# Performance work log

Measured on AMD Instinct MI355X. Metric: run time of the kernel, lower is better.

Reference implementation:

```python
import jax, jax.numpy as jnp
import numpy as np

H = 256          # hidden_channels
NP, NJ, NC = 8192, 8192, 4096  # person / job_posting / company node counts
EA, EW, EP = 262144, 131072, 131072  # edge counts per relation


def _gcn(x_src, W, b, edge_index, num_src, num_dst):
    """Bipartite GCNConv: h = x_src @ W; out[dst] = sum_e norm_e * h[src_e] + b,
    norm = deg_out(src)^-1/2 * deg_in(dst)^-1/2 (symmetric GCN normalization)."""
    h = x_src @ W                                # [num_src, H]
    row, col = edge_index[0], edge_index[1]
    ones = jnp.ones(row.shape[0], dtype=h.dtype)
    deg_src = jax.ops.segment_sum(ones, row, num_segments=num_src)
    deg_dst = jax.ops.segment_sum(ones, col, num_segments=num_dst)
    dis_src = jnp.where(deg_src > 0, jax.lax.rsqrt(jnp.maximum(deg_src, 1e-12)), 0.0)
    dis_dst = jnp.where(deg_dst > 0, jax.lax.rsqrt(jnp.maximum(deg_dst, 1e-12)), 0.0)
    norm = dis_src[row] * dis_dst[col]           # [E]
    out = jax.ops.segment_sum(h[row] * norm[:, None], col, num_segments=num_dst)
    return out + b


def setup_inputs() -> dict:
    key = jax.random.key(0)
    ks = jax.random.split(key, 12)
    s = 1.0 / np.sqrt(H)
    return {
        "x_person":  jax.random.normal(ks[0], (NP, H), jnp.float32),
        "x_job":     jax.random.normal(ks[1], (NJ, H), jnp.float32),
        "x_company": jax.random.normal(ks[2], (NC, H), jnp.float32),
        "ei_applied": jax.random.randint(ks[3], (2, EA), 0, 8192, jnp.int64 if jax.config.read('jax_enable_x64') else jnp.int32),
        "ei_worked":  jax.random.randint(ks[4], (2, EW), 0, 4096, jnp.int64 if jax.config.read('jax_enable_x64') else jnp.int32),
        "ei_posted":  jax.random.randint(ks[5], (2, EP), 0, 4096, jnp.int64 if jax.config.read('jax_enable_x64') else jnp.int32),
        "W_aj": jax.random.normal(ks[6], (H, H), jnp.float32) * s,
        "b_aj": jnp.zeros((H,), jnp.float32),
        "W_wa": jax.random.normal(ks[7], (H, H), jnp.float32) * s,
        "b_wa": jnp.zeros((H,), jnp.float32),
        "W_pb": jax.random.normal(ks[8], (H, H), jnp.float32) * s,
        "b_pb": jnp.zeros((H,), jnp.float32),
    }


def reference(x_person, x_job, x_company, ei_applied, ei_worked, ei_posted,
              W_aj, b_aj, W_wa, b_wa, W_pb, b_pb):
    Np, Nj, Nc = x_person.shape[0], x_job.shape[0], x_company.shape[0]
    # HeteroConv with aggr='sum': each dst type sums messages over its edge types
    job_emb = _gcn(x_person, W_aj, b_aj, ei_applied, Np, Nj)
    comp_emb = (_gcn(x_person, W_wa, b_wa, ei_worked, Np, Nc)
                + _gcn(x_job, W_pb, b_pb, ei_posted, Nj, Nc))  # computed but unused downstream
    del comp_emb
    person_emb = x_person  # 'person' is never a dst type; features pass through
    scores = jax.nn.sigmoid(person_emb @ job_emb.T)  # [Np, Nj]
    return scores
```

## Files before the change

### kernel.cpp

```cpp
#include <hip/hip_runtime.h>
#include <hip/hip_bf16.h>

#define HCH 256
#define NPN 8192
#define NJN 8192
#define EAE 262144

typedef _Float16 f16x8 __attribute__((ext_vector_type(8)));
typedef _Float16 f16x4 __attribute__((ext_vector_type(4)));
typedef _Float16 f16x2 __attribute__((ext_vector_type(2)));
typedef float f32x4 __attribute__((ext_vector_type(4)));

typedef __attribute__((address_space(1))) void glb_void;
typedef __attribute__((address_space(3))) void lds_void;

#define WS_DEG_SRC   0
#define WS_DEG_DST   32768
#define WS_CUR       65536
#define WS_OFFS      98304
#define WS_DIS_SRC   131328
#define WS_DIS_DST   164096
#define WS_CSR       196864
#define WS_XH        1245440
#define WS_ZH        5439744
#define WS_GH        9634048
#define WS_WHT       13828352

__global__ void k_zero(int* p) {
    int i = blockIdx.x * 256 + threadIdx.x;
    p[i] = 0;
}

__global__ void k_count(const int* __restrict__ row, const int* __restrict__ col,
                        int* deg_src, int* deg_dst) {
    int e = blockIdx.x * 256 + threadIdx.x;
    if (e < EAE) {
        atomicAdd(&deg_src[row[e]], 1);
        atomicAdd(&deg_dst[col[e]], 1);
    }
}

__global__ void k_prep(const int* __restrict__ deg_src, const int* __restrict__ deg_dst,
                       int* __restrict__ offs, float* __restrict__ dis_src,
                       float* __restrict__ dis_dst, const float* __restrict__ W,
                       _Float16* __restrict__ WhT, const float* __restrict__ x,
                       _Float16* __restrict__ Xh) {
    int bid = blockIdx.x;
    int t = threadIdx.x;
    if (bid == 0) {
        __shared__ int part[256];
        int base = t * 32;
        int local[32];
        int s = 0;
#pragma unroll
        for (int i = 0; i < 32; i++) { local[i] = s; s += deg_dst[base + i]; }
        part[t] = s;
        __syncthreads();
        for (int d = 1; d < 256; d <<= 1) {
            int self = part[t];
            int add = (t >= d) ? part[t - d] : 0;
            __syncthreads();
            part[t] = self + add;
            __syncthreads();
        }
        int chunk_excl = (t > 0) ? part[t - 1] : 0;
#pragma unroll
        for (int i = 0; i < 32; i++) offs[base + i] = chunk_excl + local[i];
        if (t == 255) offs[NJN] = part[255];
    } else if (bid < 65) {
        int i = (bid - 1) * 256 + t;
        if (i < NPN) {
            int d = deg_src[i];
            dis_src[i] = d > 0 ? rsqrtf((float)d) : 0.f;
        } else {
            int j = i - NPN;
            int d = deg_dst[j];
            dis_dst[j] = d > 0 ? rsqrtf((float)d) : 0.f;
        }
    } else if (bid < 321) {
        int idx = (bid - 65) * 256 + t;
        int n = idx >> 8, k = idx & 255;
        WhT[idx] = (_Float16)W[k * HCH + n];
    } else {
        int i = ((bid - 321) * 256 + t) * 4;
        float4 v = *(const float4*)(x + i);
        f16x4 h;
        h[0] = (_Float16)v.x; h[1] = (_Float16)v.y;
        h[2] = (_Float16)v.z; h[3] = (_Float16)v.w;
        *(f16x4*)(Xh + i) = h;
    }
}

__global__ void k_bucket(const int* __restrict__ row, const int* __restrict__ col,
                         const int* __restrict__ offs, int* cur, int* csr) {
    int e = blockIdx.x * 256 + threadIdx.x;
    if (e < EAE) {
        int c = col[e];
        int p = atomicAdd(&cur[c], 1);
        csr[offs[c] + p] = row[e];
    }
}

__global__ void k_agg(const _Float16* __restrict__ Xh, const int* __restrict__ csr,
                      const int* __restrict__ offs, const float* __restrict__ dis_src,
                      const float* __restrict__ dis_dst, _Float16* __restrict__ Zh) {
    int j = blockIdx.x;
    int c = threadIdx.x;
    int e0 = offs[j], e1 = offs[j + 1];
    float a0 = 0.f, a1 = 0.f;
    int e = e0;
    for (; e + 1 < e1; e += 2) {
        int s0 = csr[e], s1 = csr[e + 1];
        float w0 = dis_src[s0], w1 = dis_src[s1];
        f16x2 v0 = *(const f16x2*)(Xh + (size_t)s0 * HCH + 2 * c);
        f16x2 v1 = *(const f16x2*)(Xh + (size_t)s1 * HCH + 2 * c);
        a0 += w0 * (float)v0[0] + w1 * (float)v1[0];
        a1 += w0 * (float)v0[1] + w1 * (float)v1[1];
    }
    if (e < e1) {
        int s0 = csr[e];
        float w0 = dis_src[s0];
        f16x2 v0 = *(const f16x2*)(Xh + (size_t)s0 * HCH + 2 * c);
        a0 += w0 * (float)v0[0];
        a1 += w0 * (float)v0[1];
    }
    float dd = dis_dst[j];
    f16x2 out;
    out[0] = (_Float16)(a0 * dd);
    out[1] = (_Float16)(a1 * dd);
    *(f16x2*)(Zh + (size_t)j * HCH + 2 * c) = out;
}

template <bool SIGMOID>
__global__ __launch_bounds__(256, 3)
void k_gemm(const _Float16* __restrict__ A, const _Float16* __restrict__ Bt,
            const float* __restrict__ bias, void* __restrict__ Cout, int Ncols) {
    __shared__ _Float16 smA[128 * 64];
    __shared__ _Float16 smB[128 * 64];
    int tid = threadIdx.x;
    int wid = tid >> 6, lane = tid & 63;

    int bx = blockIdx.x, by = blockIdx.y;
    if (SIGMOID) {
        int nbx = gridDim.x;
        int lin = by * nbx + bx;
        int chunk = (nbx * gridDim.y) >> 3;
        int swz = (lin & 7) * chunk + (lin >> 3);
        bx = swz % nbx;
        by = swz / nbx;
    }
    int brow = by * 128;
    int bcol = bx * 128;
    int wrow = (wid >> 1) * 64;
    int wcol = (wid & 1) * 64;

    f32x4 acc[4][4] = {};

    int lr = lane & 15;
    int kq = lane >> 4;

    for (int k0 = 0; k0 < HCH; k0 += 64) {
        if (k0) __syncthreads();
#pragma unroll
        for (int i = 0; i < 4; i++) {
            int wc0 = i * 256 + wid * 64;
            int c = wc0 + lane;
            int r = c >> 3, cc = c & 7;
            const char* ga = (const char*)A +
                (size_t)(brow + r) * (HCH * 2) + (size_t)(k0 + cc * 8) * 2;
            const char* gb = (const char*)Bt +
                (size_t)(bcol + r) * (HCH * 2) + (size_t)(k0 + cc * 8) * 2;
            __builtin_amdgcn_global_load_lds(
                (glb_void*)ga, (lds_void*)((char*)smA + wc0 * 16), 16, 0, 0);
            __builtin_amdgcn_global_load_lds(
                (glb_void*)gb, (lds_void*)((char*)smB + wc0 * 16), 16, 0, 0);
        }
        __syncthreads();
#pragma unroll
        for (int kk = 0; kk < 64; kk += 32) {
            f16x8 af[4], bfr[4];
            int kbyte = (kk + kq * 8) * 2;
#pragma unroll
            for (int m = 0; m < 4; m++) {
                int r = wrow + m * 16 + lr;
                af[m] = *(const f16x8*)((const char*)smA + r * 128 + kbyte);
            }
#pragma unroll
            for (int n = 0; n < 4; n++) {
                int r = wcol + n * 16 + lr;
                bfr[n] = *(const f16x8*)((const char*)smB + r * 128 + kbyte);
            }
#pragma unroll
            for (int m = 0; m < 4; m++)
#pragma unroll
                for (int n = 0; n < 4; n++)
                    acc[m][n] = __builtin_amdgcn_mfma_f32_16x16x32_f16(
                        af[m], bfr[n], acc[m][n], 0, 0, 0);
        }
    }

    int rq = lane >> 4;
#pragma unroll
    for (int m = 0; m < 4; m++) {
#pragma unroll
        for (int n = 0; n < 4; n++) {
#pragma unroll
            for (int j = 0; j < 4; j++) {
                int gr = brow + wrow + m * 16 + rq * 4 + j;
                int gc = bcol + wcol + n * 16 + lr;
                float v = acc[m][n][j];
                if (SIGMOID) {
                    float e = __expf(-v);
                    ((float*)Cout)[(size_t)gr * Ncols + gc] =
                        __builtin_amdgcn_rcpf(1.f + e);
                } else {
                    v += bias[gc];
                    ((_Float16*)Cout)[(size_t)gr * Ncols + gc] = (_Float16)v;
                }
            }
        }
    }
}

extern "C" void kernel_launch(void* const* d_in, const int* in_sizes, int n_in,
                              void* d_out, int out_size, void* d_ws, size_t ws_size,
                              hipStream_t stream) {
    const float* x_person = (const float*)d_in[0];
    const int*   ei_app   = (const int*)d_in[3];
    const float* W_aj     = (const float*)d_in[6];
    const float* b_aj     = (const float*)d_in[7];

    const int* erow = ei_app;
    const int* ecol = ei_app + EAE;

    char* w = (char*)d_ws;
    int*   deg_src = (int*)(w + WS_DEG_SRC);
    int*   deg_dst = (int*)(w + WS_DEG_DST);
    int*   cur     = (int*)(w + WS_CUR);
    int*   offs    = (int*)(w + WS_OFFS);
    float* dis_src = (float*)(w + WS_DIS_SRC);
    float* dis_dst = (float*)(w + WS_DIS_DST);
    int*   csr     = (int*)(w + WS_CSR);
    _Float16* Xh   = (_Float16*)(w + WS_XH);
    _Float16* Zh   = (_Float16*)(w + WS_ZH);
    _Float16* Gh   = (_Float16*)(w + WS_GH);
    _Float16* WhT  = (_Float16*)(w + WS_WHT);

    k_zero<<<96, 256, 0, stream>>>((int*)w);
    k_count<<<EAE / 256, 256, 0, stream>>>(erow, ecol, deg_src, deg_dst);
    k_prep<<<2369, 256, 0, stream>>>(deg_src, deg_dst, offs, dis_src, dis_dst,
                                     W_aj, WhT, x_person, Xh);
    k_bucket<<<EAE / 256, 256, 0, stream>>>(erow, ecol, offs, cur, csr);
    k_agg<<<NJN, 128, 0, stream>>>(Xh, csr, offs, dis_src, dis_dst, Zh);
    {
        dim3 grid(HCH / 128, NJN / 128);
        k_gemm<false><<<grid, 256, 0, stream>>>(Zh, WhT, b_aj, (void*)Gh, HCH);
    }
    {
        dim3 grid(NJN / 128, NPN / 128);
        k_gemm<true><<<grid, 256, 0, stream>>>(Xh, Gh, nullptr, d_out, NJN);
    }
}
```

Measured before the change: 151.8 us.

## Double-buffer GEMM LDS tiles and template tile sizes for the small GEMM

The GEMM kernel now keeps two LDS buffers and issues the global-to-LDS loads for the next K tile before computing on the current one, so load latency overlaps with MFMA work. The kernel is templated on tile dimensions, and the Z·W GEMM uses 64x128 tiles so it launches more blocks. LDS use doubles, and launch bounds drop to 2 blocks per CU, which can lower occupancy. The final scores GEMM dominates and is likely store-bound on its 256MB fp32 output, which may limit the gain.

```diff
diff --git a/kernel.cpp b/kernel.cpp
--- a/kernel.cpp
+++ b/kernel.cpp
@@ -131,12 +131,18 @@
     *(f16x2*)(Zh + (size_t)j * HCH + 2 * c) = out;
 }
 
-template <bool SIGMOID>
-__global__ __launch_bounds__(256, 3)
+template <int TM, int TN, bool SIGMOID>
+__global__ __launch_bounds__(256, 2)
 void k_gemm(const _Float16* __restrict__ A, const _Float16* __restrict__ Bt,
             const float* __restrict__ bias, void* __restrict__ Cout, int Ncols) {
-    __shared__ _Float16 smA[128 * 64];
-    __shared__ _Float16 smB[128 * 64];
+    constexpr int WM = TM / 2, WN = TN / 2;
+    constexpr int MR = WM / 16, NR = WN / 16;
+    constexpr int CHA = TM * 8 / 256;
+    constexpr int CHB = TN * 8 / 256;
+    constexpr int BOFF = TM * 128;
+
+    __shared__ _Float16 sm[2][(TM + TN) * 64];
+
     int tid = threadIdx.x;
     int wid = tid >> 6, lane = tid & 63;
 
@@ -149,61 +155,78 @@
         bx = swz % nbx;
         by = swz / nbx;
     }
-    int brow = by * 128;
-    int bcol = bx * 128;
-    int wrow = (wid >> 1) * 64;
-    int wcol = (wid & 1) * 64;
-
-    f32x4 acc[4][4] = {};
+    int brow = by * TM;
+    int bcol = bx * TN;
+    int wrow = (wid >> 1) * WM;
+    int wcol = (wid & 1) * WN;
+
+    f32x4 acc[MR][NR] = {};
 
     int lr = lane & 15;
     int kq = lane >> 4;
 
-    for (int k0 = 0; k0 < HCH; k0 += 64) {
-        if (k0) __syncthreads();
-#pragma unroll
-        for (int i = 0; i < 4; i++) {
+    auto stage = [&](int t, int b) {
+        int k0 = t * 64;
+#pragma unroll
+        for (int i = 0; i < CHA; i++) {
             int wc0 = i * 256 + wid * 64;
             int c = wc0 + lane;
             int r = c >> 3, cc = c & 7;
             const char* ga = (const char*)A +
                 (size_t)(brow + r) * (HCH * 2) + (size_t)(k0 + cc * 8) * 2;
+            __builtin_amdgcn_global_load_lds(
+                (glb_void*)ga, (lds_void*)((char*)sm[b] + wc0 * 16), 16, 0, 0);
+        }
+#pragma unroll
+        for (int i = 0; i < CHB; i++) {
+            int wc0 = i * 256 + wid * 64;
+            int c = wc0 + lane;
+            int r = c >> 3, cc = c & 7;
             const char* gb = (const char*)Bt +
                 (size_t)(bcol + r) * (HCH * 2) + (size_t)(k0 + cc * 8) * 2;
             __builtin_amdgcn_global_load_lds(
-                (glb_void*)ga, (lds_void*)((char*)smA + wc0 * 16), 16, 0, 0);
-            __builtin_amdgcn_global_load_lds(
-                (glb_void*)gb, (lds_void*)((char*)smB + wc0 * 16), 16, 0, 0);
-        }
-        __syncthreads();
+                (glb_void*)gb, (lds_void*)((char*)sm[b] + BOFF + wc0 * 16), 16, 0, 0);
+        }
+    };
+
+    stage(0, 0);
+    __syncthreads();
+
+    constexpr int NT = HCH / 64;
+#pragma unroll
+    for (int t = 0; t < NT; t++) {
+        int cur = t & 1;
+        if (t + 1 < NT) stage(t + 1, cur ^ 1);
+        const char* base = (const char*)sm[cur];
 #pragma unroll
         for (int kk = 0; kk < 64; kk += 32) {
-            f16x8 af[4], bfr[4];
+            f16x8 af[MR], bfr[NR];
             int kbyte = (kk + kq * 8) * 2;
 #pragma unroll
-            for (int m = 0; m < 4; m++) {
+            for (int m = 0; m < MR; m++) {
                 int r = wrow + m * 16 + lr;
-                af[m] = *(const f16x8*)((const char*)smA + r * 128 + kbyte);
+                af[m] = *(const f16x8*)(base + r * 128 + kbyte);
             }
 #pragma unroll
-            for (int n = 0; n < 4; n++) {
+            for (int n = 0; n < NR; n++) {
                 int r = wcol + n * 16 + lr;
-                bfr[n] = *(const f16x8*)((const char*)smB + r * 128 + kbyte);
+                bfr[n] = *(const f16x8*)(base + BOFF + r * 128 + kbyte);
             }
 #pragma unroll
-            for (int m = 0; m < 4; m++)
-#pragma unroll
-                for (int n = 0; n < 4; n++)
+            for (int m = 0; m < MR; m++)
+#pragma unroll
+                for (int n = 0; n < NR; n++)
                     acc[m][n] = __builtin_amdgcn_mfma_f32_16x16x32_f16(
                         af[m], bfr[n], acc[m][n], 0, 0, 0);
         }
+        __syncthreads();
     }
 
     int rq = lane >> 4;
 #pragma unroll
-    for (int m = 0; m < 4; m++) {
-#pragma unroll
-        for (int n = 0; n < 4; n++) {
+    for (int m = 0; m < MR; m++) {
+#pragma unroll
+        for (int n = 0; n < NR; n++) {
 #pragma unroll
             for (int j = 0; j < 4; j++) {
                 int gr = brow + wrow + m * 16 + rq * 4 + j;
@@ -253,11 +276,11 @@
     k_bucket<<<EAE / 256, 256, 0, stream>>>(erow, ecol, offs, cur, csr);
     k_agg<<<NJN, 128, 0, stream>>>(Xh, csr, offs, dis_src, dis_dst, Zh);
     {
-        dim3 grid(HCH / 128, NJN / 128);
-        k_gemm<false><<<grid, 256, 0, stream>>>(Zh, WhT, b_aj, (void*)Gh, HCH);
+        dim3 grid(HCH / 128, NJN / 64);
+        k_gemm<64, 128, false><<<grid, 256, 0, stream>>>(Zh, WhT, b_aj, (void*)Gh, HCH);
     }
     {
         dim3 grid(NJN / 128, NPN / 128);
-        k_gemm<true><<<grid, 256, 0, stream>>>(Xh, Gh, nullptr, d_out, NJN);
-    }
-}
+        k_gemm<128, 128, true><<<grid, 256, 0, stream>>>(Xh, Gh, nullptr, d_out, NJN);
+    }
+}
```

Result: slower. 156.8 us (+3.2%).
